# Kernel optimization log

Measured on AMD Instinct MI355X. Metric: run time of the kernel, lower is better.

Reference implementation:

```python
import math
import jax, jax.numpy as jnp
import numpy as np

HEAD = 8
D_HEAD = 32
D_MODEL = 256
N = 20000
E_LOCAL = 80000
E_BOND = 60000
E_GLOBAL = 400000
MAX_DEG = 32
MAX_DIST = 64


def segment_softmax(x, seg, num_segments):
    # softmax over entries sharing the same segment id (scatter_softmax)
    m = jax.ops.segment_max(x, seg, num_segments=num_segments)
    e = jnp.exp(x - m[seg])
    s = jax.ops.segment_sum(e, seg, num_segments=num_segments)
    return e / s[seg]


def setup_inputs() -> dict:
    key = jax.random.key(0)
    ks = jax.random.split(key, 16)
    s_in = 1.0 / math.sqrt(D_MODEL)
    s_out = 1.0 / math.sqrt(2 * D_MODEL)
    dist_emb = jax.random.normal(ks[7], (MAX_DIST + 1, D_MODEL), jnp.float32) * 0.02
    dist_emb = dist_emb.at[MAX_DIST].set(0.0)  # padding_idx
    return {
        "f_node": jax.random.normal(ks[0], (N, D_MODEL), jnp.float32),
        "f_bond": jax.random.normal(ks[1], (E_BOND, D_MODEL), jnp.float32),
        "deg_matrix": jax.random.randint(ks[2], (N,), 0, MAX_DEG + 1),
        "dist_matrix": jax.random.randint(ks[3], (E_GLOBAL,), 0, MAX_DIST + 1),
        "bond_idx": jax.random.randint(ks[4], (2, E_LOCAL), 0, N),
        "query_idx": jax.random.randint(ks[5], (E_GLOBAL,), 0, N),
        "key_idx": jax.random.randint(ks[6], (E_GLOBAL,), 0, N),
        "attention_bond_idx": jnp.arange(E_BOND),
        "deg_emb": jax.random.normal(ks[8], (MAX_DEG + 1, D_MODEL), jnp.float32) * 0.02,
        "dist_emb": dist_emb,
        "Wq_w": jax.random.normal(ks[9], (D_MODEL, 2 * D_MODEL), jnp.float32) * s_in,
        "Wq_b": jnp.zeros((2 * D_MODEL,), jnp.float32),
        "Wk_w": jax.random.normal(ks[10], (D_MODEL, 2 * D_MODEL), jnp.float32) * s_in,
        "Wk_b": jnp.zeros((2 * D_MODEL,), jnp.float32),
        "Wv_w": jax.random.normal(ks[11], (D_MODEL, 2 * D_MODEL), jnp.float32) * s_in,
        "Wv_b": jnp.zeros((2 * D_MODEL,), jnp.float32),
        "out_w": jax.random.normal(ks[12], (2 * D_MODEL, D_MODEL), jnp.float32) * s_out,
        "out_b": jnp.zeros((D_MODEL,), jnp.float32),
        "bond_emb_w": jax.random.normal(ks[13], (D_MODEL, 2 * D_MODEL), jnp.float32) * s_in,
        "bond_emb_b": jnp.zeros((2 * D_MODEL,), jnp.float32),
        "bond_update_w": jax.random.normal(ks[14], (2 * D_MODEL, D_MODEL), jnp.float32) * s_out,
        "bond_update_b": jnp.zeros((D_MODEL,), jnp.float32),
    }


def reference(f_node, f_bond, deg_matrix, dist_matrix, bond_idx, query_idx, key_idx,
              attention_bond_idx, deg_emb, dist_emb, Wq_w, Wq_b, Wk_w, Wk_b, Wv_w, Wv_b,
              out_w, out_b, bond_emb_w, bond_emb_b, bond_update_w, bond_update_b):
    scale = 1.0 / math.sqrt(D_HEAD)
    n = f_node.shape[0]
    e_bond = f_bond.shape[0]

    f_deg = deg_emb[deg_matrix].reshape(n, HEAD, D_HEAD)                  # [N,H,Dh]
    ab_vb = f_bond @ bond_emb_w + bond_emb_b                               # [Eb,2D]
    attention_bond, value_bond = jnp.split(ab_vb, 2, axis=-1)
    attention_bond = attention_bond.reshape(e_bond, HEAD, D_HEAD)
    value_bond = value_bond.reshape(e_bond, HEAD, D_HEAD)
    f_dist = dist_emb[dist_matrix].reshape(-1, HEAD, D_HEAD)               # [Eg,H,Dh]

    q = (f_node @ Wq_w + Wq_b).reshape(n, 2 * HEAD, D_HEAD)
    k = (f_node @ Wk_w + Wk_b).reshape(n, 2 * HEAD, D_HEAD)
    v = (f_node @ Wv_w + Wv_b).reshape(n, 2 * HEAD, D_HEAD)
    q_local, q_global = q[:, :HEAD], q[:, HEAD:]
    k_local, k_global = k[:, :HEAD], k[:, HEAD:]
    v_local, v_global = v[:, :HEAD], v[:, HEAD:]

    src, dst = bond_idx[0], bond_idx[1]
    # ---- local (bond) attention ----
    score_local = q_local[dst] * k_local[src]                              # [El,H,Dh]
    score_local = score_local.at[:e_bond].add(attention_bond)
    score_local = score_local.sum(-1) * scale                              # [El,H]
    score_local = segment_softmax(score_local, dst, n)
    local_out = v_local[src].at[:e_bond].add(value_bond)
    local_out = local_out * score_local[:, :, None]
    local_out = jax.ops.segment_sum(local_out, dst, num_segments=n)
    local_out = local_out.reshape(n, HEAD * D_HEAD)

    # ---- global (distance) attention ----
    kg = k_global + f_deg
    score_global = q_global[query_idx] * kg[key_idx]                       # [Eg,H,Dh]
    score_global = score_global.at[attention_bond_idx].add(attention_bond)
    score_global = (score_global + f_dist).sum(-1) * scale                 # [Eg,H]
    score_global = segment_softmax(score_global, query_idx, n)
    global_out = v_global[key_idx] * score_global[:, :, None]
    global_out = jax.ops.segment_sum(global_out, query_idx, num_segments=n)
    global_out = global_out.reshape(n, HEAD * D_HEAD)

    out = jnp.concatenate([local_out, global_out], axis=-1) @ out_w + out_b  # [N,D]
    bond_out = jnp.concatenate([f_bond, out[src[:e_bond]]], axis=-1)
    bond_out = bond_out @ bond_update_w + bond_update_b                      # [Eb,D]
    return out, bond_out
```

## Files before the change

### kernel.cpp

```cpp
#include <hip/hip_runtime.h>
#include <math.h>

typedef unsigned short u16;
typedef unsigned int u32;
typedef __attribute__((ext_vector_type(8))) short s16x8;
typedef __attribute__((ext_vector_type(4))) unsigned short u16x4;
typedef __attribute__((ext_vector_type(4))) float f32x4;

__device__ __forceinline__ float bf2f(u16 x) { return __uint_as_float(((u32)x) << 16); }
__device__ __forceinline__ u16 f2bf(float f) {
    u32 u = __float_as_uint(f);
    u32 r = u + 0x7fffu + ((u >> 16) & 1u);
    return (u16)(r >> 16);
}

__device__ __forceinline__ void gll16(const u16* g, u16* l) {
    __builtin_amdgcn_global_load_lds((const __attribute__((address_space(1))) void*)g,
                                     (__attribute__((address_space(3))) void*)l,
                                     16, 0, 0);
}

template <int MODE>
__global__ __launch_bounds__(256) void gemm128(
    const u16* __restrict__ Abf, const u16* __restrict__ A2b,
    const u16* __restrict__ BT, const float* __restrict__ bias,
    u16* __restrict__ Cb, float* __restrict__ Cf, u16* __restrict__ C2b,
    const float* __restrict__ auxemb, const int* __restrict__ auxidx,
    float* __restrict__ absum, int M, int N, int K)
{
    __shared__ u16 lsA[128 * 32];
    __shared__ u16 lsB[128 * 32];

    const int tid = threadIdx.x;
    const int wave = tid >> 6;
    const int lane = tid & 63;
    const int l15 = lane & 15;
    const int quad = lane >> 4;
    const int wr = wave >> 1, wc = wave & 1;
    const int tileRow = blockIdx.y * 128;
    const int tileCol = blockIdx.x * 128;

    const int srow = tid >> 2;
    const int sk8 = (tid & 3) * 8;
    const int r0 = tileRow + srow, r1 = r0 + 64;

    const u16 *gA0, *gA1, *gA0b = nullptr, *gA1b = nullptr;
    if (MODE == 3) {
        gA0 = Abf + (size_t)r0 * 256 + sk8;
        gA1 = Abf + (size_t)r1 * 256 + sk8;
        gA0b = A2b + (size_t)auxidx[min(r0, M - 1)] * 256 + sk8;
        gA1b = A2b + (size_t)auxidx[min(r1, M - 1)] * 256 + sk8;
    } else {
        gA0 = Abf + (size_t)r0 * K + sk8;
        gA1 = Abf + (size_t)r1 * K + sk8;
    }
    const u16* gB0 = BT + (size_t)(tileCol + srow) * K + sk8;
    const u16* gB1 = BT + (size_t)(tileCol + 64 + srow) * K + sk8;

    u16* lA0 = lsA + tid * 8;
    u16* lA1 = lsA + 64 * 32 + tid * 8;
    u16* lB0 = lsB + tid * 8;
    u16* lB1 = lsB + 64 * 32 + tid * 8;

    f32x4 acc[4][4] = {};

    for (int kk = 0; kk < K; kk += 32) {
        __syncthreads();
        if (MODE == 3) {
            const u16* a0 = (kk < 256) ? gA0 + kk : gA0b + (kk - 256);
            const u16* a1 = (kk < 256) ? gA1 + kk : gA1b + (kk - 256);
            gll16(a0, lA0);
            gll16(a1, lA1);
        } else {
            gll16(gA0 + kk, lA0);
            gll16(gA1 + kk, lA1);
        }
        gll16(gB0 + kk, lB0);
        gll16(gB1 + kk, lB1);
        __syncthreads();

        s16x8 a[4], b[4];
#pragma unroll
        for (int mi = 0; mi < 4; mi++)
            a[mi] = *(const s16x8*)(lsA + (wr * 64 + mi * 16 + l15) * 32 + quad * 8);
#pragma unroll
        for (int ni = 0; ni < 4; ni++)
            b[ni] = *(const s16x8*)(lsB + (wc * 64 + ni * 16 + l15) * 32 + quad * 8);
#pragma unroll
        for (int mi = 0; mi < 4; mi++)
#pragma unroll
            for (int ni = 0; ni < 4; ni++)
                acc[mi][ni] = __builtin_amdgcn_mfma_f32_16x16x32_bf16(a[mi], b[ni],
                                                                      acc[mi][ni], 0, 0, 0);
    }

#pragma unroll
    for (int mi = 0; mi < 4; mi++) {
#pragma unroll
        for (int i = 0; i < 4; i++) {
            const int r = tileRow + wr * 64 + mi * 16 + quad * 4 + i;
            const bool rok = (r < M);
#pragma unroll
            for (int ni = 0; ni < 4; ni++) {
                const int c = tileCol + wc * 64 + ni * 16 + l15;
                float v = acc[mi][ni][i] + bias[c];
                if (MODE == 0 || MODE == 1) {
                    if (MODE == 1 && c >= 256)
                        v += auxemb[(size_t)auxidx[min(r, M - 1)] * 256 + (c - 256)];
                    if (rok) Cb[(size_t)r * N + c] = f2bf(v);
                } else if (MODE == 2) {
                    if (tileCol < 256) {
                        float s = v;
                        s += __shfl_xor(s, 1, 16);
                        s += __shfl_xor(s, 2, 16);
                        s += __shfl_xor(s, 4, 16);
                        s += __shfl_xor(s, 8, 16);
                        if (rok && l15 == 0) atomicAdd(&absum[r * 8 + (c >> 5)], s);
                    } else {
                        if (rok) Cb[(size_t)r * 256 + (c - 256)] = f2bf(v);
                    }
                } else if (MODE == 3) {
                    if (rok) Cf[(size_t)r * N + c] = v;
                } else {
                    if (rok) {
                        Cf[(size_t)r * N + c] = v;
                        C2b[(size_t)r * N + c] = f2bf(v);
                    }
                }
            }
        }
    }
}

__global__ __launch_bounds__(256) void cvt_pad(const float* __restrict__ A,
                                               u16* __restrict__ B, int M, int Mpad, int K)
{
    int t = blockIdx.x * 256 + threadIdx.x;
    if (t >= (Mpad * K) / 4) return;
    int r = (t * 4) / K;
    f32x4 v = {0.f, 0.f, 0.f, 0.f};
    if (r < M) v = *(const f32x4*)(A + (size_t)t * 4);
    u16x4 o;
#pragma unroll
    for (int j = 0; j < 4; j++) o[j] = f2bf(v[j]);
    *(u16x4*)(B + (size_t)t * 4) = o;
}

__global__ __launch_bounds__(256) void transpose_w(const float* __restrict__ B,
                                                   u16* __restrict__ BT, int K, int N)
{
    int t = blockIdx.x * 256 + threadIdx.x;
    if (t >= K * N) return;
    int n = t / K, k = t - n * K;
    BT[t] = f2bf(B[(size_t)k * N + n]);
}

__global__ __launch_bounds__(256) void rowsum32f(const float* __restrict__ E,
                                                 float* __restrict__ S, int count)
{
    int t = blockIdx.x * 256 + threadIdx.x;
    if (t >= count) return;
    const float* p = E + (size_t)t * 32;
    float s = 0.f;
#pragma unroll
    for (int j = 0; j < 32; j++) s += p[j];
    S[t] = s;
}

__global__ __launch_bounds__(256) void hist_k(const int* __restrict__ idx,
                                              int* __restrict__ cnt, int E)
{
    int e = blockIdx.x * 256 + threadIdx.x;
    if (e < E) atomicAdd(&cnt[idx[e]], 1);
}

__global__ __launch_bounds__(1024) void scan_k(const int* __restrict__ cnt,
                                               int* __restrict__ offs,
                                               int* __restrict__ cursor, int n)
{
    __shared__ int part[1024];
    const int tid = threadIdx.x;
    const int per = (n + 1023) / 1024;
    int local[32];
    int s = 0;
    for (int j = 0; j < per; j++) {
        int idx = tid * per + j;
        int c = (idx < n) ? cnt[idx] : 0;
        local[j] = s;
        s += c;
    }
    part[tid] = s;
    __syncthreads();
    for (int st = 1; st < 1024; st <<= 1) {
        int v = (tid >= st) ? part[tid - st] : 0;
        __syncthreads();
        part[tid] += v;
        __syncthreads();
    }
    int pre = (tid == 0) ? 0 : part[tid - 1];
    for (int j = 0; j < per; j++) {
        int idx = tid * per + j;
        if (idx < n) { int o = pre + local[j]; offs[idx] = o; cursor[idx] = o; }
    }
    if (tid == 1023) offs[n] = part[1023];
}

__global__ __launch_bounds__(256) void scatter_k(const int* __restrict__ idx,
                                                 int* __restrict__ cursor,
                                                 int* __restrict__ list, int E)
{
    int e = blockIdx.x * 256 + threadIdx.x;
    if (e >= E) return;
    int pos = atomicAdd(&cursor[idx[e]], 1);
    list[pos] = e;
}

template <bool GLOB>
__device__ __forceinline__ void attn_half(
    const u16* __restrict__ qb, const u16* __restrict__ kb,
    const u16* __restrict__ vbuf, const u16* __restrict__ vb,
    const int* __restrict__ offs, const int* __restrict__ lst,
    const int* __restrict__ oth, const int* __restrict__ dist,
    const float* __restrict__ absum, const float* __restrict__ distsum,
    u16* __restrict__ out, int node, int EB, float scale)
{
    const int lane = threadIdx.x & 63;
    const int head = lane >> 3;
    const int cbase = (GLOB ? 256 : 0) + lane * 4;

    const u16x4 qv = *(const u16x4*)(qb + (size_t)node * 512 + cbase);
    const float q0 = bf2f(qv[0]), q1 = bf2f(qv[1]), q2 = bf2f(qv[2]), q3 = bf2f(qv[3]);

    const int s0 = offs[node], s1 = offs[node + 1];
    float a0 = 0.f, a1 = 0.f, a2 = 0.f, a3 = 0.f, den = 0.f;
    const u16x4 zv = {0, 0, 0, 0};

#define LOADS(S, IDX)                                                          \
    {                                                                          \
        e##S = __shfl(e_l, (IDX));                                             \
        const int src = __shfl(src_l, (IDX));                                  \
        kv##S = *(const u16x4*)(kb + (size_t)src * 512 + cbase);               \
        vv##S = *(const u16x4*)(vbuf + (size_t)src * 512 + cbase);             \
        ab##S = (e##S < EB) ? absum[e##S * 8 + head] : 0.f;                    \
        if (GLOB) {                                                            \
            const int d = __shfl(d_l, (IDX));                                  \
            ds##S = distsum[d * 8 + head];                                     \
        }                                                                      \
        if (!GLOB)                                                             \
            wv##S = (e##S < EB) ? *(const u16x4*)(vb + (size_t)e##S * 256 +    \
                                                  lane * 4)                    \
                                : zv;                                          \
    }

#define COMP(S)                                                                \
    {                                                                          \
        float t = q0 * bf2f(kv##S[0]) + q1 * bf2f(kv##S[1]) +                  \
                  q2 * bf2f(kv##S[2]) + q3 * bf2f(kv##S[3]);                   \
        t += __shfl_xor(t, 1);                                                 \
        t += __shfl_xor(t, 2);                                                 \
        t += __shfl_xor(t, 4);                                                 \
        t += ab##S;                                                            \
        if (GLOB) t += ds##S;                                                  \
        const float p = __expf(t * scale);                                     \
        den += p;                                                              \
        float v0 = bf2f(vv##S[0]), v1 = bf2f(vv##S[1]);                        \
        float v2 = bf2f(vv##S[2]), v3 = bf2f(vv##S[3]);                        \
        if (!GLOB) {                                                           \
            v0 += bf2f(wv##S[0]); v1 += bf2f(wv##S[1]);                        \
            v2 += bf2f(wv##S[2]); v3 += bf2f(wv##S[3]);                        \
        }                                                                      \
        a0 += p * v0; a1 += p * v1; a2 += p * v2; a3 += p * v3;                \
    }

    for (int base = s0; base < s1; base += 64) {
        const int cnt = min(64, s1 - base);
        const int gi = base + lane;
        int e_l = 0, src_l = 0, d_l = 0;
        if (gi < s1) {
            e_l = lst[gi];
            src_l = oth[e_l];
            if (GLOB) d_l = dist[e_l];
        }

        int eX, eY;
        u16x4 kvX, vvX, wvX = zv, kvY, vvY, wvY = zv;
        float abX, dsX = 0.f, abY, dsY = 0.f;

        LOADS(X, 0);
        int i = 0;
        for (; i + 2 <= cnt; i += 2) {
            LOADS(Y, i + 1);
            COMP(X);
            if (i + 2 < cnt) LOADS(X, i + 2);
            COMP(Y);
        }
        if (i < cnt) COMP(X);
    }
#undef LOADS
#undef COMP

    const float inv = (den > 0.f) ? 1.f / den : 0.f;
    u16x4 o;
    o[0] = f2bf(a0 * inv); o[1] = f2bf(a1 * inv);
    o[2] = f2bf(a2 * inv); o[3] = f2bf(a3 * inv);
    *(u16x4*)(out + (size_t)node * 512 + cbase) = o;
}

__global__ __launch_bounds__(256) void attn_fused(
    const u16* __restrict__ qb, const u16* __restrict__ kb,
    const u16* __restrict__ vbuf, const u16* __restrict__ vb,
    const int* __restrict__ offs_l, const int* __restrict__ list_l,
    const int* __restrict__ bsrc,
    const int* __restrict__ offs_g, const int* __restrict__ list_g,
    const int* __restrict__ kidx,
    const int* __restrict__ dist, const float* __restrict__ absum,
    const float* __restrict__ distsum, u16* __restrict__ out,
    int Nn, int EB, float scale)
{
    const int w = blockIdx.x * 4 + (threadIdx.x >> 6);
    if (w >= 2 * Nn) return;
    if (w < Nn)
        attn_half<false>(qb, kb, vbuf, vb, offs_l, list_l, bsrc, dist, absum,
                         distsum, out, w, EB, scale);
    else
        attn_half<true>(qb, kb, vbuf, vb, offs_g, list_g, kidx, dist, absum,
                        distsum, out, w - Nn, EB, scale);
}

extern "C" void kernel_launch(void* const* d_in, const int* in_sizes, int n_in,
                              void* d_out, int out_size, void* d_ws, size_t ws_size,
                              hipStream_t stream)
{
    const float* f_node  = (const float*)d_in[0];
    const float* f_bond  = (const float*)d_in[1];
    const int* deg       = (const int*)d_in[2];
    const int* dist      = (const int*)d_in[3];
    const int* bond_idx  = (const int*)d_in[4];
    const int* qidx      = (const int*)d_in[5];
    const int* kidx      = (const int*)d_in[6];
    const float* deg_emb = (const float*)d_in[8];
    const float* dist_emb= (const float*)d_in[9];
    const float* Wq_w = (const float*)d_in[10]; const float* Wq_b = (const float*)d_in[11];
    const float* Wk_w = (const float*)d_in[12]; const float* Wk_b = (const float*)d_in[13];
    const float* Wv_w = (const float*)d_in[14]; const float* Wv_b = (const float*)d_in[15];
    const float* out_w = (const float*)d_in[16]; const float* out_b = (const float*)d_in[17];
    const float* be_w  = (const float*)d_in[18]; const float* be_b  = (const float*)d_in[19];
    const float* bu_w  = (const float*)d_in[20]; const float* bu_b  = (const float*)d_in[21];

    const int N_ = in_sizes[0] / 256;
    const int EB = in_sizes[1] / 256;
    const int EL = in_sizes[4] / 2;
    const int EG = in_sizes[5];
    const float scale = 0.17677669529663689f;

    const int MPN = ((N_ + 127) / 128) * 128;
    const int MPB = ((EB + 127) / 128) * 128;

    const int* bsrc = bond_idx;
    const int* bdst = bond_idx + EL;

    u16* qb   = (u16*)d_ws;
    u16* kb   = qb + (size_t)N_ * 512;
    u16* vbuf = kb + (size_t)N_ * 512;
    u16* vb   = vbuf + (size_t)N_ * 512;
    u16* wT   = vb + (size_t)EB * 256;
    u16* wqT = wT;
    u16* wkT = wT + 131072;
    u16* wvT = wT + 2 * 131072;
    u16* beT = wT + 3 * 131072;
    u16* owT = wT + 4 * 131072;
    u16* buT = wT + 5 * 131072;
    float* distsum  = (float*)(wT + 6 * 131072);
    u16* attn_out = (u16*)(distsum + 1024);
    u16* fnb      = attn_out;
    u16* fbb      = attn_out + (size_t)MPN * 512;
    u16* outb     = fbb + (size_t)MPB * 256;
    float* absum    = (float*)(outb + (size_t)N_ * 256);
    int*   cnt_l    = (int*)(absum + (size_t)EB * 8);
    int*   cnt_g    = cnt_l + N_;
    size_t zbytes   = ((size_t)EB * 8 + 2 * (size_t)N_) * 4;
    int*   offs_l   = cnt_g + N_;
    int*   offs_g   = offs_l + N_ + 4;
    int*   cur_l    = offs_g + N_ + 4;
    int*   cur_g    = cur_l + N_;
    int*   list_l   = cur_g + N_;
    int*   list_g   = list_l + EL;

    float* outp  = (float*)d_out;
    float* bondp = outp + (size_t)N_ * 256;

    hipMemsetAsync((void*)absum, 0, zbytes, stream);

    transpose_w<<<512, 256, 0, stream>>>(Wq_w, wqT, 256, 512);
    transpose_w<<<512, 256, 0, stream>>>(Wk_w, wkT, 256, 512);
    transpose_w<<<512, 256, 0, stream>>>(Wv_w, wvT, 256, 512);
    transpose_w<<<512, 256, 0, stream>>>(be_w, beT, 256, 512);
    transpose_w<<<512, 256, 0, stream>>>(out_w, owT, 512, 256);
    transpose_w<<<512, 256, 0, stream>>>(bu_w, buT, 512, 256);

    rowsum32f<<<3, 256, 0, stream>>>(dist_emb, distsum, 65 * 8);

    cvt_pad<<<(MPN * 256 / 4 + 255) / 256, 256, 0, stream>>>(f_node, fnb, N_, MPN, 256);
    cvt_pad<<<(MPB * 256 / 4 + 255) / 256, 256, 0, stream>>>(f_bond, fbb, EB, MPB, 256);

    hist_k<<<(EL + 255) / 256, 256, 0, stream>>>(bdst, cnt_l, EL);
    hist_k<<<(EG + 255) / 256, 256, 0, stream>>>(qidx, cnt_g, EG);
    scan_k<<<1, 1024, 0, stream>>>(cnt_l, offs_l, cur_l, N_);
    scan_k<<<1, 1024, 0, stream>>>(cnt_g, offs_g, cur_g, N_);
    scatter_k<<<(EL + 255) / 256, 256, 0, stream>>>(bdst, cur_l, list_l, EL);
    scatter_k<<<(EG + 255) / 256, 256, 0, stream>>>(qidx, cur_g, list_g, EG);

    dim3 g512(4, MPN / 128);
    gemm128<0><<<g512, 256, 0, stream>>>(fnb, nullptr, wqT, Wq_b, qb, nullptr, nullptr, nullptr, nullptr, nullptr, N_, 512, 256);
    gemm128<1><<<g512, 256, 0, stream>>>(fnb, nullptr, wkT, Wk_b, kb, nullptr, nullptr, deg_emb, deg, nullptr, N_, 512, 256);
    gemm128<0><<<g512, 256, 0, stream>>>(fnb, nullptr, wvT, Wv_b, vbuf, nullptr, nullptr, nullptr, nullptr, nullptr, N_, 512, 256);

    dim3 gb(4, MPB / 128);
    gemm128<2><<<gb, 256, 0, stream>>>(fbb, nullptr, beT, be_b, vb, nullptr, nullptr, nullptr, nullptr, absum, EB, 512, 256);

    attn_fused<<<(2 * N_ + 3) / 4, 256, 0, stream>>>(qb, kb, vbuf, vb,
        offs_l, list_l, bsrc, offs_g, list_g, kidx, dist, absum, distsum,
        attn_out, N_, EB, scale);

    dim3 go(2, MPN / 128);
    gemm128<4><<<go, 256, 0, stream>>>(attn_out, nullptr, owT, out_b, nullptr, outp, outb, nullptr, nullptr, nullptr, N_, 256, 512);

    dim3 gu(2, MPB / 128);
    gemm128<3><<<gu, 256, 0, stream>>>(fbb, outb, buT, bu_b, nullptr, bondp, nullptr, nullptr, bsrc, nullptr, EB, 256, 512);
}
```

Baseline: 607.3 us.

## Triple-buffer GEMM LDS with swizzle and fuse QKV projections into one launch

Replaces the synchronous load-then-compute GEMM loop with a three-stage LDS ring, using async global-to-LDS loads, explicit vmcnt waits and a single barrier per k-step. It also XOR-swizzles the LDS layout to reduce bank conflicts. The separate Q, K and V projection GEMMs become one N=1536 launch with a concatenated bias, and the degree embedding is added in the epilogue. This is meant to hide global load latency, cut launch count and improve occupancy of the grid, at the cost of three times the LDS per block, which may lower occupancy.

```diff
diff --git a/kernel.cpp b/kernel.cpp
--- a/kernel.cpp
+++ b/kernel.cpp
@@ -28,8 +28,7 @@
     const float* __restrict__ auxemb, const int* __restrict__ auxidx,
     float* __restrict__ absum, int M, int N, int K)
 {
-    __shared__ u16 lsA[128 * 32];
-    __shared__ u16 lsB[128 * 32];
+    __shared__ u16 lsmem[3 * 8192];
 
     const int tid = threadIdx.x;
     const int wave = tid >> 6;
@@ -41,7 +40,7 @@
     const int tileCol = blockIdx.x * 128;
 
     const int srow = tid >> 2;
-    const int sk8 = (tid & 3) * 8;
+    const int sk8 = (((tid & 3) ^ ((tid >> 3) & 3)) * 8);
     const int r0 = tileRow + srow, r1 = r0 + 64;
 
     const u16 *gA0, *gA1, *gA0b = nullptr, *gA1b = nullptr;
@@ -57,42 +56,62 @@
     const u16* gB0 = BT + (size_t)(tileCol + srow) * K + sk8;
     const u16* gB1 = BT + (size_t)(tileCol + 64 + srow) * K + sk8;
 
-    u16* lA0 = lsA + tid * 8;
-    u16* lA1 = lsA + 64 * 32 + tid * 8;
-    u16* lB0 = lsB + tid * 8;
-    u16* lB1 = lsB + 64 * 32 + tid * 8;
+    const int lofs = tid * 8;
+
+#define STAGE(TK, BI)                                                          \
+    {                                                                          \
+        u16* lbs = lsmem + (BI) * 8192;                                        \
+        const int kk_ = (TK) * 32;                                             \
+        if (MODE == 3) {                                                       \
+            const u16* a0 = (kk_ < 256) ? gA0 + kk_ : gA0b + (kk_ - 256);      \
+            const u16* a1 = (kk_ < 256) ? gA1 + kk_ : gA1b + (kk_ - 256);      \
+            gll16(a0, lbs + lofs);                                             \
+            gll16(a1, lbs + 2048 + lofs);                                      \
+        } else {                                                               \
+            gll16(gA0 + kk_, lbs + lofs);                                      \
+            gll16(gA1 + kk_, lbs + 2048 + lofs);                               \
+        }                                                                      \
+        gll16(gB0 + kk_, lbs + 4096 + lofs);                                   \
+        gll16(gB1 + kk_, lbs + 4096 + 2048 + lofs);                            \
+    }
 
     f32x4 acc[4][4] = {};
-
-    for (int kk = 0; kk < K; kk += 32) {
-        __syncthreads();
-        if (MODE == 3) {
-            const u16* a0 = (kk < 256) ? gA0 + kk : gA0b + (kk - 256);
-            const u16* a1 = (kk < 256) ? gA1 + kk : gA1b + (kk - 256);
-            gll16(a0, lA0);
-            gll16(a1, lA1);
-        } else {
-            gll16(gA0 + kk, lA0);
-            gll16(gA1 + kk, lA1);
+    const int nt = K >> 5;
+
+    STAGE(0, 0);
+    if (nt > 1) STAGE(1, 1);
+
+    const int xq8 = (quad ^ ((l15 >> 1) & 3)) * 8;
+    const int aoff = (wr * 64 + l15) * 32 + xq8;
+    const int boff = 4096 + (wc * 64 + l15) * 32 + xq8;
+
+    int bc = 0;
+    for (int t = 0; t < nt; ++t) {
+        if (t + 1 < nt) asm volatile("s_waitcnt vmcnt(4)" ::: "memory");
+        else            asm volatile("s_waitcnt vmcnt(0)" ::: "memory");
+        __builtin_amdgcn_s_barrier();
+        if (t + 2 < nt) {
+            const int bs = (bc >= 1) ? bc - 1 : 2;
+            STAGE(t + 2, bs);
         }
-        gll16(gB0 + kk, lB0);
-        gll16(gB1 + kk, lB1);
-        __syncthreads();
-
+
+        const u16* lb = lsmem + bc * 8192;
         s16x8 a[4], b[4];
 #pragma unroll
         for (int mi = 0; mi < 4; mi++)
-            a[mi] = *(const s16x8*)(lsA + (wr * 64 + mi * 16 + l15) * 32 + quad * 8);
+            a[mi] = *(const s16x8*)(lb + aoff + mi * 512);
 #pragma unroll
         for (int ni = 0; ni < 4; ni++)
-            b[ni] = *(const s16x8*)(lsB + (wc * 64 + ni * 16 + l15) * 32 + quad * 8);
+            b[ni] = *(const s16x8*)(lb + boff + ni * 512);
 #pragma unroll
         for (int mi = 0; mi < 4; mi++)
 #pragma unroll
             for (int ni = 0; ni < 4; ni++)
                 acc[mi][ni] = __builtin_amdgcn_mfma_f32_16x16x32_bf16(a[mi], b[ni],
                                                                       acc[mi][ni], 0, 0, 0);
-    }
+        bc = (bc == 2) ? 0 : bc + 1;
+    }
+#undef STAGE
 
 #pragma unroll
     for (int mi = 0; mi < 4; mi++) {
@@ -104,11 +123,7 @@
             for (int ni = 0; ni < 4; ni++) {
                 const int c = tileCol + wc * 64 + ni * 16 + l15;
                 float v = acc[mi][ni][i] + bias[c];
-                if (MODE == 0 || MODE == 1) {
-                    if (MODE == 1 && c >= 256)
-                        v += auxemb[(size_t)auxidx[min(r, M - 1)] * 256 + (c - 256)];
-                    if (rok) Cb[(size_t)r * N + c] = f2bf(v);
-                } else if (MODE == 2) {
+                if (MODE == 2) {
                     if (tileCol < 256) {
                         float s = v;
                         s += __shfl_xor(s, 1, 16);
@@ -121,11 +136,17 @@
                     }
                 } else if (MODE == 3) {
                     if (rok) Cf[(size_t)r * N + c] = v;
-                } else {
+                } else if (MODE == 4) {
                     if (rok) {
                         Cf[(size_t)r * N + c] = v;
                         C2b[(size_t)r * N + c] = f2bf(v);
                     }
+                } else {
+                    const int which = c >> 9;
+                    const int cc = c & 511;
+                    if (which == 1 && cc >= 256)
+                        v += auxemb[(size_t)auxidx[min(r, M - 1)] * 256 + (cc - 256)];
+                    if (rok) Cb[((size_t)which * M + r) * 512 + cc] = f2bf(v);
                 }
             }
         }
@@ -153,6 +174,17 @@
     if (t >= K * N) return;
     int n = t / K, k = t - n * K;
     BT[t] = f2bf(B[(size_t)k * N + n]);
+}
+
+__global__ __launch_bounds__(256) void concat_bias(const float* __restrict__ a,
+                                                   const float* __restrict__ b,
+                                                   const float* __restrict__ c,
+                                                   float* __restrict__ o)
+{
+    int t = blockIdx.x * 256 + threadIdx.x;
+    if (t < 512) o[t] = a[t];
+    else if (t < 1024) o[t] = b[t - 512];
+    else if (t < 1536) o[t] = c[t - 1024];
 }
 
 __global__ __launch_bounds__(256) void rowsum32f(const float* __restrict__ E,
@@ -371,7 +403,8 @@
     u16* owT = wT + 4 * 131072;
     u16* buT = wT + 5 * 131072;
     float* distsum  = (float*)(wT + 6 * 131072);
-    u16* attn_out = (u16*)(distsum + 1024);
+    float* biasC    = distsum + 1024;
+    u16* attn_out = (u16*)(biasC + 1536);
     u16* fnb      = attn_out;
     u16* fbb      = attn_out + (size_t)MPN * 512;
     u16* outb     = fbb + (size_t)MPB * 256;
@@ -397,6 +430,7 @@
     transpose_w<<<512, 256, 0, stream>>>(be_w, beT, 256, 512);
     transpose_w<<<512, 256, 0, stream>>>(out_w, owT, 512, 256);
     transpose_w<<<512, 256, 0, stream>>>(bu_w, buT, 512, 256);
+    concat_bias<<<6, 256, 0, stream>>>(Wq_b, Wk_b, Wv_b, biasC);
 
     rowsum32f<<<3, 256, 0, stream>>>(dist_emb, distsum, 65 * 8);
 
@@ -410,10 +444,8 @@
     scatter_k<<<(EL + 255) / 256, 256, 0, stream>>>(bdst, cur_l, list_l, EL);
     scatter_k<<<(EG + 255) / 256, 256, 0, stream>>>(qidx, cur_g, list_g, EG);
 
-    dim3 g512(4, MPN / 128);
-    gemm128<0><<<g512, 256, 0, stream>>>(fnb, nullptr, wqT, Wq_b, qb, nullptr, nullptr, nullptr, nullptr, nullptr, N_, 512, 256);
-    gemm128<1><<<g512, 256, 0, stream>>>(fnb, nullptr, wkT, Wk_b, kb, nullptr, nullptr, deg_emb, deg, nullptr, N_, 512, 256);
-    gemm128<0><<<g512, 256, 0, stream>>>(fnb, nullptr, wvT, Wv_b, vbuf, nullptr, nullptr, nullptr, nullptr, nullptr, N_, 512, 256);
+    dim3 g5(12, MPN / 128);
+    gemm128<5><<<g5, 256, 0, stream>>>(fnb, nullptr, wqT, biasC, qb, nullptr, nullptr, deg_emb, deg, nullptr, N_, 1536, 256);
 
     dim3 gb(4, MPB / 128);
     gemm128<2><<<gb, 256, 0, stream>>>(fbb, nullptr, beT, be_b, vb, nullptr, nullptr, nullptr, nullptr, absum, EB, 512, 256);
```

Measured after the change: 587.2 us. 1.03x faster.
